# Performance work log

Hardware: AMD Instinct MI355X
Metric: run time of the kernel (lower is better)

The kernel has to match this reference:

```python
import jax, jax.numpy as jnp
import numpy as np

IN_F, D_FC, D_H = 5, 32, 64

def setup_inputs() -> dict:
    key = jax.random.key(0)
    ks = jax.random.split(key, 10)
    B, T = 4096, 512
    s_fc = 1.0 / np.sqrt(IN_F)
    s_rnn = 1.0 / np.sqrt(D_H)
    s_out = 1.0 / np.sqrt(D_H)
    return {
        "x":    jax.random.normal(ks[0], (B, T, IN_F), dtype=jnp.float32),
        "W0":   jax.random.uniform(ks[1], (D_FC, IN_F), jnp.float32, -s_fc, s_fc),
        "b0":   jax.random.uniform(ks[2], (D_FC,), jnp.float32, -s_fc, s_fc),
        "W_ih": jax.random.uniform(ks[3], (4 * D_H, D_FC), jnp.float32, -s_rnn, s_rnn),
        "W_hh": jax.random.uniform(ks[4], (4 * D_H, D_H), jnp.float32, -s_rnn, s_rnn),
        "b_ih": jax.random.uniform(ks[5], (4 * D_H,), jnp.float32, -s_rnn, s_rnn),
        "b_hh": jax.random.uniform(ks[6], (4 * D_H,), jnp.float32, -s_rnn, s_rnn),
        "Wo":   jax.random.uniform(ks[7], (1, D_H), jnp.float32, -s_out, s_out),
        "bo":   jax.random.uniform(ks[8], (1,), jnp.float32, -s_out, s_out),
    }

def reference(x, W0, b0, W_ih, W_hh, b_ih, b_hh, Wo, bo):
    B, T, _ = x.shape
    # fc0: [B,T,5] -> [B,T,32]
    h0 = x @ W0.T + b0
    # Precompute input-side gate projections for all timesteps: [B,T,4H]
    xg = h0 @ W_ih.T + (b_ih + b_hh)
    xg_t = jnp.swapaxes(xg, 0, 1)  # [T,B,4H] for scan

    def step(carry, xg_step):
        h, c = carry
        gates = xg_step + h @ W_hh.T          # [B,4H]
        i, f, g, o = jnp.split(gates, 4, axis=-1)  # PyTorch gate order i,f,g,o
        i = jax.nn.sigmoid(i)
        f = jax.nn.sigmoid(f)
        g = jnp.tanh(g)
        o = jax.nn.sigmoid(o)
        c = f * c + i * g
        h = o * jnp.tanh(c)
        return (h, c), None

    init = (jnp.zeros((B, D_H), x.dtype), jnp.zeros((B, D_H), x.dtype))
    (h_last, _), _ = jax.lax.scan(step, init, xg_t)
    # out Linear on last timestep hidden: r_out[:, -1, :] == h_last
    return h_last @ Wo.T + bo  # [B,1]
```

## Files before the change

### kernel.cpp

```cpp
#include <hip/hip_runtime.h>

#define B_TOT   4096
#define T_STEPS 512
#define IN_F    5
#define D_FC    32
#define D_H     64
#define MB      8
#define NROW    16
#define ROWPAD  104

typedef _Float16 h8 __attribute__((ext_vector_type(8)));
typedef float    f4 __attribute__((ext_vector_type(4)));

__device__ __forceinline__ float fexp2(float x) { return __builtin_amdgcn_exp2f(x); }
__device__ __forceinline__ float frcp(float x)  { return __builtin_amdgcn_rcpf(x); }
__device__ __forceinline__ float fsig(float x) {
    return frcp(1.0f + fexp2(-1.4426950408889634f * x));
}
__device__ __forceinline__ float ftanh(float x) {
    float e = fexp2(2.8853900817779268f * x);
    return 1.0f - 2.0f * frcp(e + 1.0f);
}

__device__ __forceinline__ int mrow(int b) { return ((b >> 1) << 2) | (b & 1); }

__global__ __launch_bounds__(256) void lstm_mfma(
    const float* __restrict__ x,
    const float* __restrict__ W0,
    const float* __restrict__ b0,
    const float* __restrict__ W_ih,
    const float* __restrict__ W_hh,
    const float* __restrict__ b_ih,
    const float* __restrict__ b_hh,
    const float* __restrict__ Wo,
    const float* __restrict__ bo,
    float* __restrict__ out)
{
    __shared__ _Float16 H[2][NROW][ROWPAD];

    const int tid  = threadIdx.x;
    const int lane = tid & 63;
    const int w    = tid >> 6;
    const int col  = lane & 15;
    const int quad = lane >> 4;
    const int bblk = blockIdx.x * MB;

    h8 Bf[4][3];
    #pragma unroll
    for (int q = 0; q < 4; ++q) {
        const int row = q * 64 + w * 16 + col;
        #pragma unroll
        for (int c = 0; c < 3; ++c) {
            h8 f;
            #pragma unroll
            for (int jj = 0; jj < 8; ++jj) {
                const int k = c * 32 + quad * 8 + jj;
                const float wv = (k < D_FC) ? W_ih[row * D_FC + k]
                                            : W_hh[row * D_H + (k - D_FC)];
                f[jj] = (_Float16)wv;
            }
            Bf[q][c] = f;
        }
    }
    float bias_q[4];
    #pragma unroll
    for (int q = 0; q < 4; ++q) {
        const int row = q * 64 + w * 16 + col;
        bias_q[q] = b_ih[row] + b_hh[row];
    }

    const int fb = tid >> 5;
    const int fc = tid & 31;
    const int frow = mrow(fb);
    float w0c[IN_F], b0s;
    #pragma unroll
    for (int i = 0; i < IN_F; ++i) w0c[i] = W0[fc * IN_F + i];
    b0s = b0[fc];

    const float* xb = x + (size_t)(bblk + fb) * T_STEPS * IN_F;

    #pragma unroll
    for (int p = 0; p < 2; ++p) {
        H[p][frow][D_FC + fc]      = (_Float16)0.0f;
        H[p][frow][2 * D_FC + fc]  = (_Float16)0.0f;
        const int grow = frow + 2;
        H[p][grow][fc]             = (_Float16)0.0f;
        H[p][grow][D_FC + fc]      = (_Float16)0.0f;
        H[p][grow][2 * D_FC + fc]  = (_Float16)0.0f;
    }
    {
        float a = b0s;
        #pragma unroll
        for (int i = 0; i < IN_F; ++i) a = fmaf(w0c[i], xb[i], a);
        H[0][frow][fc] = (_Float16)a;
    }
    float xr[IN_F];
    #pragma unroll
    for (int i = 0; i < IN_F; ++i) xr[i] = xb[IN_F + i];

    float c_st[2] = {0.0f, 0.0f};

    __syncthreads();

    for (int t = 0; t < T_STEPS; ++t) {
        const int rp = t & 1, wp = rp ^ 1;

        const h8 A0 = *(const h8*)&H[rp][col][quad * 8];
        const h8 A1 = *(const h8*)&H[rp][col][32 + quad * 8];
        const h8 A2 = *(const h8*)&H[rp][col][64 + quad * 8];

        f4 acc[4];
        #pragma unroll
        for (int q = 0; q < 4; ++q) {
            f4 a = { bias_q[q], bias_q[q], bias_q[q], bias_q[q] };
            a = __builtin_amdgcn_mfma_f32_16x16x32_f16(A0, Bf[q][0], a, 0, 0, 0);
            a = __builtin_amdgcn_mfma_f32_16x16x32_f16(A1, Bf[q][1], a, 0, 0, 0);
            a = __builtin_amdgcn_mfma_f32_16x16x32_f16(A2, Bf[q][2], a, 0, 0, 0);
            acc[q] = a;
        }

        #pragma unroll
        for (int r = 0; r < 2; ++r) {
            const float ig = fsig(acc[0][r]);
            const float fg = fsig(acc[1][r]);
            const float g_ = ftanh(acc[2][r]);
            const float og = fsig(acc[3][r]);
            c_st[r] = fmaf(fg, c_st[r], ig * g_);
            const float hh = og * ftanh(c_st[r]);
            H[wp][quad * 4 + r][D_FC + w * 16 + col] = (_Float16)hh;
        }

        {
            float a = b0s;
            #pragma unroll
            for (int i = 0; i < IN_F; ++i) a = fmaf(w0c[i], xr[i], a);
            H[wp][frow][fc] = (_Float16)a;
        }
        const int tn = (t + 2 < T_STEPS) ? (t + 2) : (T_STEPS - 1);
        #pragma unroll
        for (int i = 0; i < IN_F; ++i) xr[i] = xb[tn * IN_F + i];

        __syncthreads();
    }

    if (tid < MB) {
        const int hr = mrow(tid);
        float a = bo[0];
        #pragma unroll 8
        for (int j = 0; j < D_H; ++j)
            a = fmaf((float)H[0][hr][D_FC + j], Wo[j], a);
        out[bblk + tid] = a;
    }
}

extern "C" void kernel_launch(void* const* d_in, const int* in_sizes, int n_in,
                              void* d_out, int out_size, void* d_ws, size_t ws_size,
                              hipStream_t stream) {
    const float* x    = (const float*)d_in[0];
    const float* W0   = (const float*)d_in[1];
    const float* b0   = (const float*)d_in[2];
    const float* W_ih = (const float*)d_in[3];
    const float* W_hh = (const float*)d_in[4];
    const float* b_ih = (const float*)d_in[5];
    const float* b_hh = (const float*)d_in[6];
    const float* Wo   = (const float*)d_in[7];
    const float* bo   = (const float*)d_in[8];
    float* out = (float*)d_out;

    hipLaunchKernelGGL(lstm_mfma, dim3(B_TOT / MB), dim3(256), 0, stream,
                       x, W0, b0, W_ih, W_hh, b_ih, b_hh, Wo, bo, out);
}
```

Baseline: 338.2 us.

## Halve batches per block to one MFMA row per lane and fold bias into exponent

Each block now handles 4 batch rows instead of 8, placed on MFMA rows 0,4,8,12, so each lane evaluates the gate activations for a single row per timestep. The grid doubles and launch bounds request 4 blocks per CU, so more waves are available to hide the latency of the serial per-step chain. Gate biases are pre-scaled and folded into the exp2 argument with an fma, so the MFMA accumulator starts from zero. In exchange, the total number of MFMA instructions doubles because three quarters of the 16 A-rows are now padding.

```diff
diff --git a/kernel.cpp b/kernel.cpp
--- a/kernel.cpp
+++ b/kernel.cpp
@@ -5,26 +5,20 @@
 #define IN_F    5
 #define D_FC    32
 #define D_H     64
-#define MB      8
+#define MB      4
 #define NROW    16
 #define ROWPAD  104
 
 typedef _Float16 h8 __attribute__((ext_vector_type(8)));
 typedef float    f4 __attribute__((ext_vector_type(4)));
 
+#define LOG2E    1.4426950408889634f
+#define TWOLOG2E 2.8853900817779268f
+
 __device__ __forceinline__ float fexp2(float x) { return __builtin_amdgcn_exp2f(x); }
 __device__ __forceinline__ float frcp(float x)  { return __builtin_amdgcn_rcpf(x); }
-__device__ __forceinline__ float fsig(float x) {
-    return frcp(1.0f + fexp2(-1.4426950408889634f * x));
-}
-__device__ __forceinline__ float ftanh(float x) {
-    float e = fexp2(2.8853900817779268f * x);
-    return 1.0f - 2.0f * frcp(e + 1.0f);
-}
 
-__device__ __forceinline__ int mrow(int b) { return ((b >> 1) << 2) | (b & 1); }
-
-__global__ __launch_bounds__(256) void lstm_mfma(
+__global__ __launch_bounds__(256, 4) void lstm_mfma(
     const float* __restrict__ x,
     const float* __restrict__ W0,
     const float* __restrict__ b0,
@@ -62,43 +56,46 @@
             Bf[q][c] = f;
         }
     }
-    float bias_q[4];
-    #pragma unroll
-    for (int q = 0; q < 4; ++q) {
-        const int row = q * 64 + w * 16 + col;
-        bias_q[q] = b_ih[row] + b_hh[row];
+    float bs_i, bs_f, bt_g, bs_o;
+    {
+        const int r0 = 0 * 64 + w * 16 + col;
+        const int r1 = 1 * 64 + w * 16 + col;
+        const int r2 = 2 * 64 + w * 16 + col;
+        const int r3 = 3 * 64 + w * 16 + col;
+        bs_i = -LOG2E    * (b_ih[r0] + b_hh[r0]);
+        bs_f = -LOG2E    * (b_ih[r1] + b_hh[r1]);
+        bt_g =  TWOLOG2E * (b_ih[r2] + b_hh[r2]);
+        bs_o = -LOG2E    * (b_ih[r3] + b_hh[r3]);
     }
 
-    const int fb = tid >> 5;
-    const int fc = tid & 31;
-    const int frow = mrow(fb);
+    const int fc = lane & 31;
     float w0c[IN_F], b0s;
     #pragma unroll
     for (int i = 0; i < IN_F; ++i) w0c[i] = W0[fc * IN_F + i];
     b0s = b0[fc];
 
-    const float* xb = x + (size_t)(bblk + fb) * T_STEPS * IN_F;
+    const float* xb = x + (size_t)(bblk + w) * T_STEPS * IN_F;
 
-    #pragma unroll
-    for (int p = 0; p < 2; ++p) {
-        H[p][frow][D_FC + fc]      = (_Float16)0.0f;
-        H[p][frow][2 * D_FC + fc]  = (_Float16)0.0f;
-        const int grow = frow + 2;
-        H[p][grow][fc]             = (_Float16)0.0f;
-        H[p][grow][D_FC + fc]      = (_Float16)0.0f;
-        H[p][grow][2 * D_FC + fc]  = (_Float16)0.0f;
+    for (int i = tid; i < 2 * NROW * 96; i += 256) {
+        const int p  = i / (NROW * 96);
+        const int rr = (i / 96) % NROW;
+        const int cc = i % 96;
+        H[p][rr][cc] = (_Float16)0.0f;
     }
+    __syncthreads();
+
     {
         float a = b0s;
         #pragma unroll
         for (int i = 0; i < IN_F; ++i) a = fmaf(w0c[i], xb[i], a);
-        H[0][frow][fc] = (_Float16)a;
+        if (lane < 32) H[0][4 * w][fc] = (_Float16)a;
     }
     float xr[IN_F];
     #pragma unroll
     for (int i = 0; i < IN_F; ++i) xr[i] = xb[IN_F + i];
 
-    float c_st[2] = {0.0f, 0.0f};
+    float c_st = 0.0f;
+    const f4 zero4 = {0.0f, 0.0f, 0.0f, 0.0f};
 
     __syncthreads();
 
@@ -112,29 +109,33 @@
         f4 acc[4];
         #pragma unroll
         for (int q = 0; q < 4; ++q) {
-            f4 a = { bias_q[q], bias_q[q], bias_q[q], bias_q[q] };
-            a = __builtin_amdgcn_mfma_f32_16x16x32_f16(A0, Bf[q][0], a, 0, 0, 0);
+            f4 a = __builtin_amdgcn_mfma_f32_16x16x32_f16(A0, Bf[q][0], zero4, 0, 0, 0);
             a = __builtin_amdgcn_mfma_f32_16x16x32_f16(A1, Bf[q][1], a, 0, 0, 0);
             a = __builtin_amdgcn_mfma_f32_16x16x32_f16(A2, Bf[q][2], a, 0, 0, 0);
             acc[q] = a;
         }
 
-        #pragma unroll
-        for (int r = 0; r < 2; ++r) {
-            const float ig = fsig(acc[0][r]);
-            const float fg = fsig(acc[1][r]);
-            const float g_ = ftanh(acc[2][r]);
-            const float og = fsig(acc[3][r]);
-            c_st[r] = fmaf(fg, c_st[r], ig * g_);
-            const float hh = og * ftanh(c_st[r]);
-            H[wp][quad * 4 + r][D_FC + w * 16 + col] = (_Float16)hh;
+        {
+            const float ei = fexp2(fmaf(-LOG2E,    acc[0][0], bs_i));
+            const float ii = frcp(1.0f + ei);
+            const float ef = fexp2(fmaf(-LOG2E,    acc[1][0], bs_f));
+            const float ff = frcp(1.0f + ef);
+            const float eg = fexp2(fmaf(TWOLOG2E,  acc[2][0], bt_g));
+            const float g_ = fmaf(-2.0f, frcp(1.0f + eg), 1.0f);
+            const float eo = fexp2(fmaf(-LOG2E,    acc[3][0], bs_o));
+            const float oo = frcp(1.0f + eo);
+            c_st = fmaf(ff, c_st, ii * g_);
+            const float ec = fexp2(TWOLOG2E * c_st);
+            const float th = fmaf(-2.0f, frcp(1.0f + ec), 1.0f);
+            const float hh = oo * th;
+            H[wp][4 * quad][D_FC + w * 16 + col] = (_Float16)hh;
         }
 
         {
             float a = b0s;
             #pragma unroll
             for (int i = 0; i < IN_F; ++i) a = fmaf(w0c[i], xr[i], a);
-            H[wp][frow][fc] = (_Float16)a;
+            if (lane < 32) H[wp][4 * w][fc] = (_Float16)a;
         }
         const int tn = (t + 2 < T_STEPS) ? (t + 2) : (T_STEPS - 1);
         #pragma unroll
@@ -144,11 +145,10 @@
     }
 
     if (tid < MB) {
-        const int hr = mrow(tid);
         float a = bo[0];
         #pragma unroll 8
         for (int j = 0; j < D_H; ++j)
-            a = fmaf((float)H[0][hr][D_FC + j], Wo[j], a);
+            a = fmaf((float)H[0][4 * tid][D_FC + j], Wo[j], a);
         out[bblk + tid] = a;
     }
 }
```

Result: slower. 448.6 us (+32.7%).

## Process two independent batch groups per block with interleaved MFMA chains

Applied to the files above, without the earlier changes.

Each block now handles two groups of 8 sequences, interleaving their MFMA chains and gate math so the two independent dependency chains can hide each other's latency. This halves the grid size and the per-step barrier count per sequence. Bias is pre-scaled and folded into the exp2 argument with an fma instead of seeding the accumulator, and LDS is zeroed with a simple loop. Fewer blocks (256) may underfill the CUs, and register pressure rises.

```diff
diff --git a/kernel.cpp b/kernel.cpp
--- a/kernel.cpp
+++ b/kernel.cpp
@@ -5,26 +5,23 @@
 #define IN_F    5
 #define D_FC    32
 #define D_H     64
-#define MB      8
+#define NG      2
+#define GB      8
 #define NROW    16
 #define ROWPAD  104
 
 typedef _Float16 h8 __attribute__((ext_vector_type(8)));
 typedef float    f4 __attribute__((ext_vector_type(4)));
 
+#define LOG2E    1.4426950408889634f
+#define TWOLOG2E 2.8853900817779268f
+
 __device__ __forceinline__ float fexp2(float x) { return __builtin_amdgcn_exp2f(x); }
 __device__ __forceinline__ float frcp(float x)  { return __builtin_amdgcn_rcpf(x); }
-__device__ __forceinline__ float fsig(float x) {
-    return frcp(1.0f + fexp2(-1.4426950408889634f * x));
-}
-__device__ __forceinline__ float ftanh(float x) {
-    float e = fexp2(2.8853900817779268f * x);
-    return 1.0f - 2.0f * frcp(e + 1.0f);
-}
 
 __device__ __forceinline__ int mrow(int b) { return ((b >> 1) << 2) | (b & 1); }
 
-__global__ __launch_bounds__(256) void lstm_mfma(
+__global__ __launch_bounds__(256, 1) void lstm_mfma(
     const float* __restrict__ x,
     const float* __restrict__ W0,
     const float* __restrict__ b0,
@@ -36,14 +33,14 @@
     const float* __restrict__ bo,
     float* __restrict__ out)
 {
-    __shared__ _Float16 H[2][NROW][ROWPAD];
+    __shared__ _Float16 H[NG][2][NROW][ROWPAD];
 
     const int tid  = threadIdx.x;
     const int lane = tid & 63;
     const int w    = tid >> 6;
     const int col  = lane & 15;
     const int quad = lane >> 4;
-    const int bblk = blockIdx.x * MB;
+    const int bblk = blockIdx.x * (NG * GB);
 
     h8 Bf[4][3];
     #pragma unroll
@@ -62,94 +59,120 @@
             Bf[q][c] = f;
         }
     }
-    float bias_q[4];
+    float bsc[4];
     #pragma unroll
     for (int q = 0; q < 4; ++q) {
         const int row = q * 64 + w * 16 + col;
-        bias_q[q] = b_ih[row] + b_hh[row];
+        const float bf = b_ih[row] + b_hh[row];
+        bsc[q] = (q == 2) ? TWOLOG2E * bf : -LOG2E * bf;
     }
 
-    const int fb = tid >> 5;
-    const int fc = tid & 31;
+    const int fb   = tid >> 5;
+    const int fc   = tid & 31;
     const int frow = mrow(fb);
-    float w0c[IN_F], b0s;
+    float w0c[IN_F];
     #pragma unroll
     for (int i = 0; i < IN_F; ++i) w0c[i] = W0[fc * IN_F + i];
-    b0s = b0[fc];
+    const float b0s = b0[fc];
 
-    const float* xb = x + (size_t)(bblk + fb) * T_STEPS * IN_F;
+    const float* xA = x + (size_t)(bblk + fb) * T_STEPS * IN_F;
+    const float* xB = x + (size_t)(bblk + GB + fb) * T_STEPS * IN_F;
 
+    {
+        unsigned* p = (unsigned*)&H[0][0][0][0];
+        const int ndw = NG * 2 * NROW * ROWPAD / 2;
+        for (int i = tid; i < ndw; i += 256) p[i] = 0u;
+    }
+    __syncthreads();
+    {
+        float a = b0s, b = b0s;
+        #pragma unroll
+        for (int i = 0; i < IN_F; ++i) {
+            a = fmaf(w0c[i], xA[i], a);
+            b = fmaf(w0c[i], xB[i], b);
+        }
+        H[0][0][frow][fc] = (_Float16)a;
+        H[1][0][frow][fc] = (_Float16)b;
+    }
+    float xrA[IN_F], xrB[IN_F];
     #pragma unroll
-    for (int p = 0; p < 2; ++p) {
-        H[p][frow][D_FC + fc]      = (_Float16)0.0f;
-        H[p][frow][2 * D_FC + fc]  = (_Float16)0.0f;
-        const int grow = frow + 2;
-        H[p][grow][fc]             = (_Float16)0.0f;
-        H[p][grow][D_FC + fc]      = (_Float16)0.0f;
-        H[p][grow][2 * D_FC + fc]  = (_Float16)0.0f;
-    }
-    {
-        float a = b0s;
-        #pragma unroll
-        for (int i = 0; i < IN_F; ++i) a = fmaf(w0c[i], xb[i], a);
-        H[0][frow][fc] = (_Float16)a;
-    }
-    float xr[IN_F];
-    #pragma unroll
-    for (int i = 0; i < IN_F; ++i) xr[i] = xb[IN_F + i];
+    for (int i = 0; i < IN_F; ++i) { xrA[i] = xA[IN_F + i]; xrB[i] = xB[IN_F + i]; }
 
-    float c_st[2] = {0.0f, 0.0f};
+    float cA[2] = {0.0f, 0.0f}, cB[2] = {0.0f, 0.0f};
+    const f4 zero4 = {0.0f, 0.0f, 0.0f, 0.0f};
 
     __syncthreads();
 
     for (int t = 0; t < T_STEPS; ++t) {
         const int rp = t & 1, wp = rp ^ 1;
 
-        const h8 A0 = *(const h8*)&H[rp][col][quad * 8];
-        const h8 A1 = *(const h8*)&H[rp][col][32 + quad * 8];
-        const h8 A2 = *(const h8*)&H[rp][col][64 + quad * 8];
+        const h8 A0 = *(const h8*)&H[0][rp][col][quad * 8];
+        const h8 A1 = *(const h8*)&H[0][rp][col][32 + quad * 8];
+        const h8 A2 = *(const h8*)&H[0][rp][col][64 + quad * 8];
+        const h8 B0 = *(const h8*)&H[1][rp][col][quad * 8];
+        const h8 B1 = *(const h8*)&H[1][rp][col][32 + quad * 8];
+        const h8 B2 = *(const h8*)&H[1][rp][col][64 + quad * 8];
 
-        f4 acc[4];
+        f4 accA[4], accB[4];
         #pragma unroll
         for (int q = 0; q < 4; ++q) {
-            f4 a = { bias_q[q], bias_q[q], bias_q[q], bias_q[q] };
-            a = __builtin_amdgcn_mfma_f32_16x16x32_f16(A0, Bf[q][0], a, 0, 0, 0);
+            f4 a = __builtin_amdgcn_mfma_f32_16x16x32_f16(A0, Bf[q][0], zero4, 0, 0, 0);
+            f4 b = __builtin_amdgcn_mfma_f32_16x16x32_f16(B0, Bf[q][0], zero4, 0, 0, 0);
             a = __builtin_amdgcn_mfma_f32_16x16x32_f16(A1, Bf[q][1], a, 0, 0, 0);
+            b = __builtin_amdgcn_mfma_f32_16x16x32_f16(B1, Bf[q][1], b, 0, 0, 0);
             a = __builtin_amdgcn_mfma_f32_16x16x32_f16(A2, Bf[q][2], a, 0, 0, 0);
-            acc[q] = a;
+            b = __builtin_amdgcn_mfma_f32_16x16x32_f16(B2, Bf[q][2], b, 0, 0, 0);
+            accA[q] = a; accB[q] = b;
         }
 
         #pragma unroll
         for (int r = 0; r < 2; ++r) {
-            const float ig = fsig(acc[0][r]);
-            const float fg = fsig(acc[1][r]);
-            const float g_ = ftanh(acc[2][r]);
-            const float og = fsig(acc[3][r]);
-            c_st[r] = fmaf(fg, c_st[r], ig * g_);
-            const float hh = og * ftanh(c_st[r]);
-            H[wp][quad * 4 + r][D_FC + w * 16 + col] = (_Float16)hh;
+            const float iiA = frcp(1.0f + fexp2(fmaf(-LOG2E,   accA[0][r], bsc[0])));
+            const float ffA = frcp(1.0f + fexp2(fmaf(-LOG2E,   accA[1][r], bsc[1])));
+            const float ggA = fmaf(-2.0f, frcp(1.0f + fexp2(fmaf(TWOLOG2E, accA[2][r], bsc[2]))), 1.0f);
+            const float ooA = frcp(1.0f + fexp2(fmaf(-LOG2E,   accA[3][r], bsc[3])));
+            cA[r] = fmaf(ffA, cA[r], iiA * ggA);
+            const float thA = fmaf(-2.0f, frcp(1.0f + fexp2(TWOLOG2E * cA[r])), 1.0f);
+            H[0][wp][quad * 4 + r][D_FC + w * 16 + col] = (_Float16)(ooA * thA);
+
+            const float iiB = frcp(1.0f + fexp2(fmaf(-LOG2E,   accB[0][r], bsc[0])));
+            const float ffB = frcp(1.0f + fexp2(fmaf(-LOG2E,   accB[1][r], bsc[1])));
+            const float ggB = fmaf(-2.0f, frcp(1.0f + fexp2(fmaf(TWOLOG2E, accB[2][r], bsc[2]))), 1.0f);
+            const float ooB = frcp(1.0f + fexp2(fmaf(-LOG2E,   accB[3][r], bsc[3])));
+            cB[r] = fmaf(ffB, cB[r], iiB * ggB);
+            const float thB = fmaf(-2.0f, frcp(1.0f + fexp2(TWOLOG2E * cB[r])), 1.0f);
+            H[1][wp][quad * 4 + r][D_FC + w * 16 + col] = (_Float16)(ooB * thB);
         }
 
         {
-            float a = b0s;
+            float a = b0s, b = b0s;
             #pragma unroll
-            for (int i = 0; i < IN_F; ++i) a = fmaf(w0c[i], xr[i], a);
-            H[wp][frow][fc] = (_Float16)a;
+            for (int i = 0; i < IN_F; ++i) {
+                a = fmaf(w0c[i], xrA[i], a);
+                b = fmaf(w0c[i], xrB[i], b);
+            }
+            H[0][wp][frow][fc] = (_Float16)a;
+            H[1][wp][frow][fc] = (_Float16)b;
         }
         const int tn = (t + 2 < T_STEPS) ? (t + 2) : (T_STEPS - 1);
         #pragma unroll
-        for (int i = 0; i < IN_F; ++i) xr[i] = xb[tn * IN_F + i];
+        for (int i = 0; i < IN_F; ++i) {
+            xrA[i] = xA[tn * IN_F + i];
+            xrB[i] = xB[tn * IN_F + i];
+        }
 
         __syncthreads();
     }
 
-    if (tid < MB) {
-        const int hr = mrow(tid);
+    if (tid < NG * GB) {
+        const int g  = tid >> 3;
+        const int b  = tid & 7;
+        const int hr = mrow(b);
         float a = bo[0];
         #pragma unroll 8
         for (int j = 0; j < D_H; ++j)
-            a = fmaf((float)H[0][hr][D_FC + j], Wo[j], a);
-        out[bblk + tid] = a;
+            a = fmaf((float)H[g][0][hr][D_FC + j], Wo[j], a);
+        out[bblk + g * GB + b] = a;
     }
 }
 
@@ -167,6 +190,6 @@
     const float* bo   = (const float*)d_in[8];
     float* out = (float*)d_out;
 
-    hipLaunchKernelGGL(lstm_mfma, dim3(B_TOT / MB), dim3(256), 0, stream,
+    hipLaunchKernelGGL(lstm_mfma, dim3(B_TOT / (NG * GB)), dim3(256), 0, stream,
                        x, W0, b0, W_ih, W_hh, b_ih, b_hh, Wo, bo, out);
 }
```

Result: slower. 398.1 us (+17.7%).

## Halve batch per block to 4 rows using 2 waves covering 32 hidden units each

Applied to the files above, without the earlier changes.

Each block now handles 4 batch rows with 128 threads (2 waves), and each wave computes two 16-column groups per gate, so it issues twice the MFMAs and holds twice the weight fragments. The grid doubles to 1024 blocks, which spreads the serial recurrence across more CUs, and launch bounds ask for 2 blocks per SIMD. Bias is pre-scaled and folded into the exp2 argument through an fma, removing a multiply from each gate activation. The trade is more register pressure per thread and heavier MFMA waste, since only 4 of the 16 MFMA rows carry real data.

```diff
diff --git a/kernel.cpp b/kernel.cpp
--- a/kernel.cpp
+++ b/kernel.cpp
@@ -5,26 +5,20 @@
 #define IN_F    5
 #define D_FC    32
 #define D_H     64
-#define MB      8
+#define MB      4
 #define NROW    16
 #define ROWPAD  104
 
 typedef _Float16 h8 __attribute__((ext_vector_type(8)));
 typedef float    f4 __attribute__((ext_vector_type(4)));
 
+#define LOG2E    1.4426950408889634f
+#define TWOLOG2E 2.8853900817779268f
+
 __device__ __forceinline__ float fexp2(float x) { return __builtin_amdgcn_exp2f(x); }
 __device__ __forceinline__ float frcp(float x)  { return __builtin_amdgcn_rcpf(x); }
-__device__ __forceinline__ float fsig(float x) {
-    return frcp(1.0f + fexp2(-1.4426950408889634f * x));
-}
-__device__ __forceinline__ float ftanh(float x) {
-    float e = fexp2(2.8853900817779268f * x);
-    return 1.0f - 2.0f * frcp(e + 1.0f);
-}
 
-__device__ __forceinline__ int mrow(int b) { return ((b >> 1) << 2) | (b & 1); }
-
-__global__ __launch_bounds__(256) void lstm_mfma(
+__global__ __launch_bounds__(128, 2) void lstm_mfma(
     const float* __restrict__ x,
     const float* __restrict__ W0,
     const float* __restrict__ b0,
@@ -45,60 +39,64 @@
     const int quad = lane >> 4;
     const int bblk = blockIdx.x * MB;
 
-    h8 Bf[4][3];
+    h8 Bf[4][2][3];
     #pragma unroll
     for (int q = 0; q < 4; ++q) {
-        const int row = q * 64 + w * 16 + col;
         #pragma unroll
-        for (int c = 0; c < 3; ++c) {
-            h8 f;
+        for (int jg = 0; jg < 2; ++jg) {
+            const int n = q * 64 + w * 32 + jg * 16 + col;
             #pragma unroll
-            for (int jj = 0; jj < 8; ++jj) {
-                const int k = c * 32 + quad * 8 + jj;
-                const float wv = (k < D_FC) ? W_ih[row * D_FC + k]
-                                            : W_hh[row * D_H + (k - D_FC)];
-                f[jj] = (_Float16)wv;
+            for (int c = 0; c < 3; ++c) {
+                h8 f;
+                #pragma unroll
+                for (int jj = 0; jj < 8; ++jj) {
+                    const int k = c * 32 + quad * 8 + jj;
+                    const float wv = (k < D_FC) ? W_ih[n * D_FC + k]
+                                                : W_hh[n * D_H + (k - D_FC)];
+                    f[jj] = (_Float16)wv;
+                }
+                Bf[q][jg][c] = f;
             }
-            Bf[q][c] = f;
         }
     }
-    float bias_q[4];
+    float bsc[4][2];
     #pragma unroll
-    for (int q = 0; q < 4; ++q) {
-        const int row = q * 64 + w * 16 + col;
-        bias_q[q] = b_ih[row] + b_hh[row];
-    }
+    for (int q = 0; q < 4; ++q)
+        #pragma unroll
+        for (int jg = 0; jg < 2; ++jg) {
+            const int n = q * 64 + w * 32 + jg * 16 + col;
+            const float bf = b_ih[n] + b_hh[n];
+            bsc[q][jg] = (q == 2) ? TWOLOG2E * bf : -LOG2E * bf;
+        }
 
     const int fb = tid >> 5;
     const int fc = tid & 31;
-    const int frow = mrow(fb);
-    float w0c[IN_F], b0s;
+    float w0c[IN_F];
     #pragma unroll
     for (int i = 0; i < IN_F; ++i) w0c[i] = W0[fc * IN_F + i];
-    b0s = b0[fc];
+    const float b0s = b0[fc];
 
     const float* xb = x + (size_t)(bblk + fb) * T_STEPS * IN_F;
 
-    #pragma unroll
-    for (int p = 0; p < 2; ++p) {
-        H[p][frow][D_FC + fc]      = (_Float16)0.0f;
-        H[p][frow][2 * D_FC + fc]  = (_Float16)0.0f;
-        const int grow = frow + 2;
-        H[p][grow][fc]             = (_Float16)0.0f;
-        H[p][grow][D_FC + fc]      = (_Float16)0.0f;
-        H[p][grow][2 * D_FC + fc]  = (_Float16)0.0f;
+    {
+        unsigned* p = (unsigned*)&H[0][0][0];
+        #pragma unroll
+        for (int i = 0; i < 13; ++i)
+            p[tid + 128 * i] = 0u;
     }
+    __syncthreads();
     {
         float a = b0s;
         #pragma unroll
         for (int i = 0; i < IN_F; ++i) a = fmaf(w0c[i], xb[i], a);
-        H[0][frow][fc] = (_Float16)a;
+        H[0][4 * fb][fc] = (_Float16)a;
     }
     float xr[IN_F];
     #pragma unroll
     for (int i = 0; i < IN_F; ++i) xr[i] = xb[IN_F + i];
 
     float c_st[2] = {0.0f, 0.0f};
+    const f4 zero4 = {0.0f, 0.0f, 0.0f, 0.0f};
 
     __syncthreads();
 
@@ -109,32 +107,33 @@
         const h8 A1 = *(const h8*)&H[rp][col][32 + quad * 8];
         const h8 A2 = *(const h8*)&H[rp][col][64 + quad * 8];
 
-        f4 acc[4];
+        f4 acc[4][2];
         #pragma unroll
-        for (int q = 0; q < 4; ++q) {
-            f4 a = { bias_q[q], bias_q[q], bias_q[q], bias_q[q] };
-            a = __builtin_amdgcn_mfma_f32_16x16x32_f16(A0, Bf[q][0], a, 0, 0, 0);
-            a = __builtin_amdgcn_mfma_f32_16x16x32_f16(A1, Bf[q][1], a, 0, 0, 0);
-            a = __builtin_amdgcn_mfma_f32_16x16x32_f16(A2, Bf[q][2], a, 0, 0, 0);
-            acc[q] = a;
-        }
+        for (int q = 0; q < 4; ++q)
+            #pragma unroll
+            for (int jg = 0; jg < 2; ++jg) {
+                f4 a = __builtin_amdgcn_mfma_f32_16x16x32_f16(A0, Bf[q][jg][0], zero4, 0, 0, 0);
+                a = __builtin_amdgcn_mfma_f32_16x16x32_f16(A1, Bf[q][jg][1], a, 0, 0, 0);
+                a = __builtin_amdgcn_mfma_f32_16x16x32_f16(A2, Bf[q][jg][2], a, 0, 0, 0);
+                acc[q][jg] = a;
+            }
 
         #pragma unroll
-        for (int r = 0; r < 2; ++r) {
-            const float ig = fsig(acc[0][r]);
-            const float fg = fsig(acc[1][r]);
-            const float g_ = ftanh(acc[2][r]);
-            const float og = fsig(acc[3][r]);
-            c_st[r] = fmaf(fg, c_st[r], ig * g_);
-            const float hh = og * ftanh(c_st[r]);
-            H[wp][quad * 4 + r][D_FC + w * 16 + col] = (_Float16)hh;
+        for (int jg = 0; jg < 2; ++jg) {
+            const float ii = frcp(1.0f + fexp2(fmaf(-LOG2E,   acc[0][jg][0], bsc[0][jg])));
+            const float ff = frcp(1.0f + fexp2(fmaf(-LOG2E,   acc[1][jg][0], bsc[1][jg])));
+            const float g_ = fmaf(-2.0f, frcp(1.0f + fexp2(fmaf(TWOLOG2E, acc[2][jg][0], bsc[2][jg]))), 1.0f);
+            const float oo = frcp(1.0f + fexp2(fmaf(-LOG2E,   acc[3][jg][0], bsc[3][jg])));
+            c_st[jg] = fmaf(ff, c_st[jg], ii * g_);
+            const float th = fmaf(-2.0f, frcp(1.0f + fexp2(TWOLOG2E * c_st[jg])), 1.0f);
+            H[wp][4 * quad][D_FC + w * 32 + jg * 16 + col] = (_Float16)(oo * th);
         }
 
         {
             float a = b0s;
             #pragma unroll
             for (int i = 0; i < IN_F; ++i) a = fmaf(w0c[i], xr[i], a);
-            H[wp][frow][fc] = (_Float16)a;
+            H[wp][4 * fb][fc] = (_Float16)a;
         }
         const int tn = (t + 2 < T_STEPS) ? (t + 2) : (T_STEPS - 1);
         #pragma unroll
@@ -144,11 +143,10 @@
     }
 
     if (tid < MB) {
-        const int hr = mrow(tid);
         float a = bo[0];
         #pragma unroll 8
         for (int j = 0; j < D_H; ++j)
-            a = fmaf((float)H[0][hr][D_FC + j], Wo[j], a);
+            a = fmaf((float)H[0][4 * tid][D_FC + j], Wo[j], a);
         out[bblk + tid] = a;
     }
 }
@@ -167,6 +165,6 @@
     const float* bo   = (const float*)d_in[8];
     float* out = (float*)d_out;
 
-    hipLaunchKernelGGL(lstm_mfma, dim3(B_TOT / MB), dim3(256), 0, stream,
+    hipLaunchKernelGGL(lstm_mfma, dim3(B_TOT / MB), dim3(128), 0, stream,
                        x, W0, b0, W_ih, W_hh, b_ih, b_hh, Wo, bo, out);
 }
```

New measurement: 431.5 us. 27.6% more time.
